# Kernel tuning notes

Measured on AMD Instinct MI355X. Metric: run time of the kernel, lower is better.

## Reference

```python
import jax, jax.numpy as jnp
import numpy as np

H = 64; DS = 32; DT = 24; ED = 16; OUT = 2
N = 10000       # nodes per type
E = 40000       # edges per edge type (before self loops)
MAX_DEG = 12    # static padded neighbor-sequence length (PyG to_dense_batch max); excess dropped


def setup_inputs() -> dict:
    key = jax.random.key(0)
    k = iter(jax.random.split(key, 40))
    def lin(o, i):
        s = 1.0 / np.sqrt(i)
        return jax.random.uniform(next(k), (o, i), jnp.float32, -s, s)
    inp = {}
    inp["x_source"] = jax.random.normal(next(k), (N, DS), jnp.float32)
    inp["x_target"] = jax.random.normal(next(k), (N, DT), jnp.float32)
    # 4 edge types in order [src->src, tgt->tgt, src->tgt, tgt->src], each [2, E]
    inp["edges"] = jax.random.randint(next(k), (4, 2, E), 0, N, dtype=jnp.int32)
    inp["edge_attr_st"] = jax.random.normal(next(k), (E, ED), jnp.float32)
    # node encoders (Linear-ReLU-Dropout(eval)-Linear)
    inp["We_s1"] = lin(H, DS); inp["be_s1"] = jnp.zeros((H,), jnp.float32)
    inp["We_s2"] = lin(H, H);  inp["be_s2"] = jnp.zeros((H,), jnp.float32)
    inp["We_t1"] = lin(H, DT); inp["be_t1"] = jnp.zeros((H,), jnp.float32)
    inp["We_t2"] = lin(H, H);  inp["be_t2"] = jnp.zeros((H,), jnp.float32)
    # 12 SAGEConv(aggr='lstm') blocks: 3 layers x 4 edge types, stacked on dim 0
    s = 1.0 / np.sqrt(H)
    inp["Wih"] = jax.random.uniform(next(k), (12, 4 * H, H), jnp.float32, -s, s)
    inp["Whh"] = jax.random.uniform(next(k), (12, 4 * H, H), jnp.float32, -s, s)
    inp["bih"] = jax.random.uniform(next(k), (12, 4 * H), jnp.float32, -s, s)
    inp["bhh"] = jax.random.uniform(next(k), (12, 4 * H), jnp.float32, -s, s)
    inp["Wl"]  = jax.random.uniform(next(k), (12, H, H), jnp.float32, -s, s)
    inp["bl"]  = jnp.zeros((12, H), jnp.float32)
    inp["Wr"]  = jax.random.uniform(next(k), (12, H, H), jnp.float32, -s, s)
    # edge gate + edge MLP head
    inp["Wg1"] = lin(H, 2 * H);   inp["bg1"] = jnp.zeros((H,), jnp.float32)
    inp["Wg2"] = lin(1, H);       inp["bg2"] = jnp.zeros((1,), jnp.float32)
    inp["Wm1"] = lin(H, H + ED);  inp["bm1"] = jnp.zeros((H,), jnp.float32)
    inp["Wm2"] = lin(H // 2, H);  inp["bm2"] = jnp.zeros((H // 2,), jnp.float32)
    inp["Wm3"] = lin(OUT, H // 2); inp["bm3"] = jnp.zeros((OUT,), jnp.float32)
    return inp


def _lstm_last(dense, Wih, Whh, bih, bhh):
    # dense: [n, T, H] padded neighbor sequences; PyG LSTMAggregation returns lstm(x)[0][:, -1]
    n = dense.shape[0]
    h0 = jnp.zeros((n, H), dense.dtype)
    def step(carry, x_t):
        h, c = carry
        g = x_t @ Wih.T + bih + h @ Whh.T + bhh  # torch gate order: i, f, g, o
        i, f, gg, o = jnp.split(g, 4, axis=-1)
        c = jax.nn.sigmoid(f) * c + jax.nn.sigmoid(i) * jnp.tanh(gg)
        h = jax.nn.sigmoid(o) * jnp.tanh(c)
        return (h, c), None
    (h, _), _ = jax.lax.scan(step, (h0, h0), jnp.swapaxes(dense, 0, 1))
    return h


def _sage_lstm(x_src, x_dst, src, dst, Wih, Whh, bih, bhh, Wl, bl, Wr):
    n_src, n_dst = x_src.shape[0], x_dst.shape[0]
    # add_self_loops(num_nodes=n_dst): appends (i, i) for every destination node, zero edge_attr
    loop = jnp.arange(n_dst, dtype=src.dtype)
    src = jnp.concatenate([src, loop]); dst = jnp.concatenate([dst, loop])
    # sort_edge_index(sort_by_row=False): stable lexicographic (dst, src) order
    order = jnp.argsort(dst.astype(jnp.int64) * n_src + src.astype(jnp.int64))
    src_s, dst_s = src[order], dst[order]
    xj = x_src[src_s]                                   # gather neighbor feats [E', H]
    deg = jnp.zeros((n_dst,), jnp.int32).at[dst_s].add(1)
    start = jnp.cumsum(deg) - deg                       # CSR row starts
    pos = jnp.arange(dst_s.shape[0], dtype=jnp.int32) - start[dst_s]
    dense = jnp.zeros((n_dst, MAX_DEG, x_src.shape[1]), x_src.dtype)
    dense = dense.at[dst_s, pos].set(xj, mode="drop")   # pad-to-dense, drop beyond MAX_DEG
    agg = _lstm_last(dense, Wih, Whh, bih, bhh)
    # SAGEConv: lin_l(aggr) + lin_r(x_root); lin_r has no bias
    return agg @ Wl.T + bl + x_dst @ Wr.T


def reference(x_source, x_target, edges, edge_attr_st,
              We_s1, be_s1, We_s2, be_s2, We_t1, be_t1, We_t2, be_t2,
              Wih, Whh, bih, bhh, Wl, bl, Wr,
              Wg1, bg1, Wg2, bg2, Wm1, bm1, Wm2, bm2, Wm3, bm3):
    relu = jax.nn.relu
    xs = relu(x_source @ We_s1.T + be_s1) @ We_s2.T + be_s2
    xt = relu(x_target @ We_t1.T + be_t1) @ We_t2.T + be_t2

    def layer(xs, xt, L):
        specs = [(xs, xs, 0), (xt, xt, 1), (xs, xt, 2), (xt, xs, 3)]
        outs = []
        for x_src, x_dst, et in specs:
            i = L * 4 + et
            outs.append(_sage_lstm(x_src, x_dst, edges[et, 0], edges[et, 1],
                                   Wih[i], Whh[i], bih[i], bhh[i], Wl[i], bl[i], Wr[i]))
        # HeteroConv(aggr='mean'): each node type receives from exactly 2 edge types
        return 0.5 * (outs[0] + outs[3]), 0.5 * (outs[1] + outs[2])

    s1, t1 = layer(xs, xt, 0); s1, t1 = relu(s1), relu(t1)
    s2, t2 = layer(s1, t1, 1); s2, t2 = relu(s2 + s1), relu(t2 + t1)
    s3, t3 = layer(s2, t2, 2); s3, t3 = relu(s3 + s2), relu(t3 + t2)

    # edge head on the main ('source','to','target') edges (original edges, no self loops)
    se, te = s3[edges[2, 0]], t3[edges[2, 1]]
    g = jax.nn.sigmoid(relu(jnp.concatenate([se, te], -1) @ Wg1.T + bg1) @ Wg2.T + bg2)
    er = g * se + (1.0 - g) * te
    h = relu(jnp.concatenate([er, edge_attr_st], -1) @ Wm1.T + bm1)
    h = relu(h @ Wm2.T + bm2)
    return h @ Wm3.T + bm3  # [E, OUT] edge logits
```

## Files before the change

kernel.cpp:

```cpp
#include <hip/hip_runtime.h>

#define N_NODES 10000
#define N_EDGES 40000
#define HD 64
#define MAXD 12
#define CAP 32
#define YROW ((size_t)(N_NODES + 1) * 256)
#define LOG2E 1.44269504f
#define XST 148

typedef __attribute__((ext_vector_type(8))) short short8;
typedef __attribute__((ext_vector_type(4))) float floatx4;

#define MFMA16(A, B, C) __builtin_amdgcn_mfma_f32_16x16x32_bf16(A, B, C, 0, 0, 0)

#if __has_builtin(__builtin_amdgcn_exp2f)
#define EXP2(x) __builtin_amdgcn_exp2f(x)
#else
#define EXP2(x) __expf((x) * 0.6931471806f)
#endif

__device__ __forceinline__ float sigmoidf_(float x) {
  return 1.0f / (1.0f + __expf(-x));
}
__device__ __forceinline__ float fma4(float4 w, float4 x, float a) {
  a = fmaf(w.x, x.x, a);
  a = fmaf(w.y, x.y, a);
  a = fmaf(w.z, x.z, a);
  return fmaf(w.w, x.w, a);
}

__device__ __forceinline__ void split_frag(float4 a, float4 b, short8& hi, short8& lo) {
  float f[8] = {a.x, a.y, a.z, a.w, b.x, b.y, b.z, b.w};
  union { short8 v; unsigned d[4]; } H, L;
#pragma unroll
  for (int p = 0; p < 4; ++p) {
    unsigned u0 = __float_as_uint(f[2 * p]);
    unsigned u1 = __float_as_uint(f[2 * p + 1]);
    H.d[p] = (u0 >> 16) | (u1 & 0xFFFF0000u);
    float l0 = f[2 * p] - __uint_as_float(u0 & 0xFFFF0000u);
    float l1 = f[2 * p + 1] - __uint_as_float(u1 & 0xFFFF0000u);
    L.d[p] = (__float_as_uint(l0) >> 16) | (__float_as_uint(l1) & 0xFFFF0000u);
  }
  hi = H.v;
  lo = L.v;
}


__global__ void scatter_kernel(const int* __restrict__ edges, int* __restrict__ cnt,
                               int* __restrict__ pool) {
  int idx = blockIdx.x * 256 + threadIdx.x;
  if (idx >= 4 * N_EDGES) return;
  int et = idx / N_EDGES, e = idx - et * N_EDGES;
  int src = edges[(et * 2) * N_EDGES + e];
  int dst = edges[(et * 2 + 1) * N_EDGES + e];
  int slot = atomicAdd(&cnt[et * N_NODES + dst], 1);
  if (slot < CAP) pool[(et * N_NODES + dst) * CAP + slot] = src;
}

__global__ void sortrows_kernel(const int* __restrict__ cnt, const int* __restrict__ pool,
                                int* __restrict__ nbr) {
  __shared__ int buf[64][CAP + 1];
  int idx = blockIdx.x * 64 + threadIdx.x;
  if (idx >= 4 * N_NODES) return;
  int n = idx % N_NODES;
  int c = cnt[idx];
  if (c > CAP) c = CAP;
  int* a = buf[threadIdx.x];
  const int* row = pool + idx * CAP;
  for (int j = 0; j < c; ++j) a[j] = row[j] * 2;
  a[c] = n * 2 + 1;
  ++c;
  for (int i2 = 1; i2 < c; ++i2) {
    int key = a[i2];
    int b = i2 - 1;
    while (b >= 0 && a[b] > key) { a[b + 1] = a[b]; --b; }
    a[b + 1] = key;
  }
  int* onbr = nbr + idx * MAXD;
  for (int t = 0; t < MAXD; ++t) onbr[t] = (t < c) ? (a[t] >> 1) : N_NODES;
}


__device__ __forceinline__ void wfrag_body(const float* __restrict__ W,
                                           short* __restrict__ w16, int gid) {
  int lane = gid & 63;
  int combo = gid >> 6;
  int kc = combo & 1;
  int g = (combo >> 1) & 3;
  int w = (combo >> 3) & 3;
  int i = combo >> 5;
  float sc = (g == 2) ? (2.0f * LOG2E) : LOG2E;
  int gate = g * 64 + w * 16 + (lane & 15);
  int k0 = kc * 32 + (lane >> 4) * 8;
  const float* src = W + ((size_t)i * 256 + gate) * 64 + k0;
  float4 a = ((const float4*)src)[0];
  float4 b = ((const float4*)src)[1];
  a.x *= sc; a.y *= sc; a.z *= sc; a.w *= sc;
  b.x *= sc; b.y *= sc; b.z *= sc; b.w *= sc;
  short8 hi, lo;
  split_frag(a, b, hi, lo);
  short8* dst = (short8*)w16;
  dst[(combo * 2 + 0) * 64 + lane] = hi;
  dst[(combo * 2 + 1) * 64 + lane] = lo;
}

__device__ __forceinline__ void cw_body(const float* __restrict__ Wl,
    const float* __restrict__ Wr, short* __restrict__ cw, int gid) {
  int lane = gid & 63;
  int rest = gid >> 6;
  int combo = rest & 7;
  int mat = (rest >> 3) % 3;
  int pair = rest / 24;
  int L = pair >> 1, side = pair & 1;
  int iA = L * 4 + (side ? 1 : 0);
  int iB = L * 4 + (side ? 2 : 3);
  int wp = combo >> 1, kc = combo & 1;
  int row = wp * 16 + (lane & 15);
  int k0 = kc * 32 + (lane >> 4) * 8;
  float4 a, b;
  if (mat == 0) {
    const float* s = Wl + ((size_t)iA * 64 + row) * 64 + k0;
    a = ((const float4*)s)[0]; b = ((const float4*)s)[1];
  } else if (mat == 1) {
    const float* s = Wl + ((size_t)iB * 64 + row) * 64 + k0;
    a = ((const float4*)s)[0]; b = ((const float4*)s)[1];
  } else {
    const float* sA = Wr + ((size_t)iA * 64 + row) * 64 + k0;
    const float* sB = Wr + ((size_t)iB * 64 + row) * 64 + k0;
    float4 a1 = ((const float4*)sA)[0], b1 = ((const float4*)sA)[1];
    float4 a2 = ((const float4*)sB)[0], b2 = ((const float4*)sB)[1];
    a.x = a1.x + a2.x; a.y = a1.y + a2.y; a.z = a1.z + a2.z; a.w = a1.w + a2.w;
    b.x = b1.x + b2.x; b.y = b1.y + b2.y; b.z = b1.z + b2.z; b.w = b1.w + b2.w;
  }
  short8 hi, lo;
  split_frag(a, b, hi, lo);
  short8* dst = (short8*)cw;
  int base = ((pair * 3 + mat) * 8 + combo) * 2;
  dst[(base + 0) * 64 + lane] = hi;
  dst[(base + 1) * 64 + lane] = lo;
}

__device__ __forceinline__ void eh_body(const float* __restrict__ Wg1,
    const float* __restrict__ Wm1, const float* __restrict__ Wm2,
    short* __restrict__ ehw16, int gid) {
  int lane = gid & 63;
  int combo = gid >> 6;
  int n = lane & 15, quad = lane >> 4;
  int mat, wp, kc;
  if (combo < 16) { mat = 0; wp = combo >> 2; kc = combo & 3; }
  else if (combo < 28) { int c2 = combo - 16; mat = 1; wp = c2 / 3; kc = c2 % 3; }
  else { int c2 = combo - 28; mat = 2; wp = c2 >> 1; kc = c2 & 1; }
  int row = wp * 16 + n;
  int k0 = kc * 32 + quad * 8;
  float4 a = {0.f, 0.f, 0.f, 0.f}, b = {0.f, 0.f, 0.f, 0.f};
  if (mat == 0) {
    const float* s = Wg1 + (size_t)row * 128 + k0;
    a = ((const float4*)s)[0]; b = ((const float4*)s)[1];
  } else if (mat == 1) {
    if (k0 + 8 <= 80) {
      const float* s = Wm1 + (size_t)row * 80 + k0;
      a = ((const float4*)s)[0]; b = ((const float4*)s)[1];
    }
  } else {
    const float* s = Wm2 + (size_t)row * 64 + k0;
    a = ((const float4*)s)[0]; b = ((const float4*)s)[1];
  }
  short8 hi, lo;
  split_frag(a, b, hi, lo);
  short8* dst = (short8*)ehw16;
  dst[(combo * 2 + 0) * 64 + lane] = hi;
  dst[(combo * 2 + 1) * 64 + lane] = lo;
}

__global__ __launch_bounds__(256) void prep_all_kernel(
    const float* __restrict__ Whh, const float* __restrict__ Wih,
    const float* __restrict__ Wl, const float* __restrict__ Wr,
    const float* __restrict__ Wg1, const float* __restrict__ Wm1,
    const float* __restrict__ Wm2,
    short* __restrict__ whh16, short* __restrict__ wih16, short* __restrict__ cw16,
    short* __restrict__ ehw16, float* __restrict__ ybase) {
  int gid = blockIdx.x * 256 + threadIdx.x;
  if (gid < 24576) {
    wfrag_body(Whh, whh16, gid);
  } else if (gid < 49152) {
    wfrag_body(Wih, wih16, gid - 24576);
  } else if (gid < 58368) {
    cw_body(Wl, Wr, cw16, gid - 49152);
  } else if (gid < 60416) {
    eh_body(Wg1, Wm1, Wm2, ehw16, gid - 58368);
  } else if (gid < 61440) {
    int t = gid - 60416;
    int et = t >> 8, col = t & 255;
    ybase[(size_t)et * YROW + (size_t)N_NODES * 256 + col] = 0.0f;
  }
}


template <int IN>
__device__ __forceinline__ void encode_body(const float* __restrict__ x,
    const float* __restrict__ W1, const float* __restrict__ b1,
    const float* __restrict__ W2, const float* __restrict__ b2, float* __restrict__ out) {
  __shared__ float xs[4][IN];
  __shared__ float h1[4][HD];
  int w = threadIdx.x >> 6, l = threadIdx.x & 63;
  int n = blockIdx.x * 4 + w;
  if (l < IN) xs[w][l] = x[n * IN + l];
  __syncthreads();
  float acc = b1[l];
#pragma unroll
  for (int k = 0; k < IN; ++k) acc = fmaf(xs[w][k], W1[l * IN + k], acc);
  h1[w][l] = fmaxf(acc, 0.0f);
  __syncthreads();
  float acc2 = b2[l];
#pragma unroll
  for (int k = 0; k < HD; ++k) acc2 = fmaf(h1[w][k], W2[l * HD + k], acc2);
  out[n * HD + l] = acc2;
}

__global__ __launch_bounds__(256) void encode_both_kernel(
    const float* __restrict__ xs0, const float* __restrict__ xt0,
    const float* __restrict__ Ws1, const float* __restrict__ bs1,
    const float* __restrict__ Ws2, const float* __restrict__ bs2,
    const float* __restrict__ Wt1, const float* __restrict__ bt1,
    const float* __restrict__ Wt2, const float* __restrict__ bt2,
    float* __restrict__ outS, float* __restrict__ outT) {
  if (blockIdx.y == 0) encode_body<32>(xs0, Ws1, bs1, Ws2, bs2, outS);
  else encode_body<24>(xt0, Wt1, bt1, Wt2, bt2, outT);
}


__global__ __launch_bounds__(256) void ygemm_mfma_kernel(const float* __restrict__ xs0,
    const float* __restrict__ xt0, const short* __restrict__ wih16L, float* __restrict__ ybase) {
  __shared__ __align__(16) float xS[16][68];
  __shared__ __align__(16) float pS[16][260];
  int et = blockIdx.y;
  const float* x = (et == 0 || et == 2) ? xs0 : xt0;
  const short8* wf = (const short8*)(wih16L + (size_t)et * 32768);
  float* y = ybase + (size_t)et * YROW;
  int tid = threadIdx.x, w = tid >> 6, l = tid & 63;
  int quad = l >> 4, n = l & 15;
  int n0 = blockIdx.x * 16;
  {
    int node = tid >> 4, f4 = tid & 15;
    float4 v = *(const float4*)(x + (size_t)(n0 + node) * 64 + f4 * 4);
    *(float4*)&xS[node][f4 * 4] = v;
  }
  short8 Bh[4][2], Bl[4][2];
#pragma unroll
  for (int wp = 0; wp < 4; ++wp)
#pragma unroll
    for (int kc = 0; kc < 2; ++kc) {
      int combo = (wp * 4 + w) * 2 + kc;
      Bh[wp][kc] = wf[(combo * 2 + 0) * 64 + l];
      Bl[wp][kc] = wf[(combo * 2 + 1) * 64 + l];
    }
  __syncthreads();
  short8 Ah[2], Al[2];
  {
    const float* hp = &xS[n][quad * 8];
    float4 q0 = *(const float4*)hp, q1 = *(const float4*)(hp + 4);
    float4 q2 = *(const float4*)(hp + 32), q3 = *(const float4*)(hp + 36);
    split_frag(q0, q1, Ah[0], Al[0]);
    split_frag(q2, q3, Ah[1], Al[1]);
  }
  floatx4 acc[4];
#pragma unroll
  for (int wp = 0; wp < 4; ++wp) {
    floatx4 a = {0.f, 0.f, 0.f, 0.f};
    a = MFMA16(Ah[0], Bh[wp][0], a);
    a = MFMA16(Ah[1], Bh[wp][1], a);
    a = MFMA16(Al[0], Bh[wp][0], a);
    a = MFMA16(Al[1], Bh[wp][1], a);
    a = MFMA16(Ah[0], Bl[wp][0], a);
    a = MFMA16(Ah[1], Bl[wp][1], a);
    acc[wp] = a;
  }
#pragma unroll
  for (int wp = 0; wp < 4; ++wp)
#pragma unroll
    for (int r = 0; r < 4; ++r)
      pS[quad * 4 + r][(wp * 16 + n) * 4 + w] = acc[wp][r];
  __syncthreads();
#pragma unroll
  for (int cc = 0; cc < 4; ++cc) {
    int g4 = cc * 256 + tid;
    int node = g4 >> 6, col = g4 & 63;
    float4 v = *(const float4*)&pS[node][col * 4];
    ((float4*)(y + (size_t)(n0 + node) * 256))[col] = v;
  }
}


__global__ __launch_bounds__(256) void lstm_mfma_kernel(const int* __restrict__ nbrAll,
    const float* __restrict__ ybase, const short* __restrict__ whh16L,
    const float* __restrict__ bihL, const float* __restrict__ bhhL, float* __restrict__ aggBase) {
  __shared__ __align__(16) unsigned pkS[2][16 * 68];
  __shared__ int nbS[16][MAXD];
  int et = blockIdx.y;
  const int* nbr = nbrAll + (size_t)et * N_NODES * MAXD;
  const float4* y4 = (const float4*)(ybase + (size_t)et * YROW);
  const short* whh16 = whh16L + (size_t)et * 32768;
  const float* bih = bihL + et * 256;
  const float* bhh = bhhL + et * 256;
  float* agg = aggBase + (size_t)et * N_NODES * HD;
  int tid = threadIdx.x, w = tid >> 6, l = tid & 63;
  int quad = l >> 4, n = l & 15, u = w * 16 + n;
  int n0 = blockIdx.x * 16;
  if (tid < 16 * MAXD) ((int*)nbS)[tid] = nbr[n0 * MAXD + tid];
  short8 Bh[4][2], Bl[4][2];
  {
    const short8* wf = (const short8*)whh16;
#pragma unroll
    for (int g = 0; g < 4; ++g)
#pragma unroll
      for (int kc = 0; kc < 2; ++kc) {
        int combo = (w * 4 + g) * 2 + kc;
        Bh[g][kc] = wf[(combo * 2 + 0) * 64 + l];
        Bl[g][kc] = wf[(combo * 2 + 1) * 64 + l];
      }
  }
  float bs[4];
#pragma unroll
  for (int g = 0; g < 4; ++g)
    bs[g] = (bih[g * 64 + u] + bhh[g * 64 + u]) * ((g == 2) ? (2.0f * LOG2E) : LOG2E);
  float c[4] = {0.f, 0.f, 0.f, 0.f}, h[4];
  short8 Ah[2], Al[2];
#pragma unroll
  for (int kc = 0; kc < 2; ++kc) { Ah[kc] = (short8)0; Al[kc] = (short8)0; }
  __syncthreads();
  float4 Y[4];
#pragma unroll
  for (int r = 0; r < 4; ++r) Y[r] = y4[(size_t)nbS[quad * 4 + r][0] * 64 + u];
  for (int t = 0; t < MAXD; ++t) {
    float yg[4][4];
#pragma unroll
    for (int r = 0; r < 4; ++r) {
      yg[0][r] = Y[r].x; yg[1][r] = Y[r].y; yg[2][r] = Y[r].z; yg[3][r] = Y[r].w;
    }
    floatx4 acc[4];
#pragma unroll
    for (int g = 0; g < 4; ++g) {
      floatx4 a = {yg[g][0], yg[g][1], yg[g][2], yg[g][3]};
      a = MFMA16(Ah[0], Bh[g][0], a);
      a = MFMA16(Ah[1], Bh[g][1], a);
      a = MFMA16(Al[0], Bh[g][0], a);
      a = MFMA16(Al[1], Bh[g][1], a);
      a = MFMA16(Ah[0], Bl[g][0], a);
      a = MFMA16(Ah[1], Bl[g][1], a);
      acc[g] = a;
    }
    if (t + 1 < MAXD) {
#pragma unroll
      for (int r = 0; r < 4; ++r) Y[r] = y4[(size_t)nbS[quad * 4 + r][t + 1] * 64 + u];
    }
    int buf = (t + 1) & 1;
#pragma unroll
    for (int r = 0; r < 4; ++r) {
      float gi = acc[0][r] + bs[0];
      float gf = acc[1][r] + bs[1];
      float gg = acc[2][r] + bs[2];
      float go = acc[3][r] + bs[3];
      float a_ = EXP2(-gi);
      float b_ = EXP2(fminf(-gg, 60.f));
      float f_ = EXP2(-gf);
      float o_ = EXP2(-go);
      float p1 = 1.f + a_, p2 = 1.f + b_, p3 = 1.f + f_;
      float d1 = p1 * p2;
      float num = fmaf(c[r], d1, (1.f - b_) * p3);
      c[r] = num * __builtin_amdgcn_rcpf(p3 * d1);
      float e_ = EXP2(c[r] * (-2.0f * LOG2E));
      h[r] = (1.f - e_) * __builtin_amdgcn_rcpf((1.f + e_) * (1.f + o_));
      unsigned ub = __float_as_uint(h[r]);
      float lo = h[r] - __uint_as_float(ub & 0xFFFF0000u);
      pkS[buf][(quad * 4 + r) * 68 + u] =
          __builtin_amdgcn_perm(ub, __float_as_uint(lo), 0x07060302u);
    }
    __syncthreads();
    if (t + 1 < MAXD) {
#pragma unroll
      for (int kc = 0; kc < 2; ++kc) {
        const unsigned* pb = &pkS[buf][n * 68 + kc * 32 + quad * 8];
        uint4 qa = *(const uint4*)pb;
        uint4 qb = *(const uint4*)(pb + 4);
        union { short8 s; unsigned d[4]; } H, L;
        H.d[0] = __builtin_amdgcn_perm(qa.y, qa.x, 0x07060302u);
        H.d[1] = __builtin_amdgcn_perm(qa.w, qa.z, 0x07060302u);
        H.d[2] = __builtin_amdgcn_perm(qb.y, qb.x, 0x07060302u);
        H.d[3] = __builtin_amdgcn_perm(qb.w, qb.z, 0x07060302u);
        L.d[0] = __builtin_amdgcn_perm(qa.y, qa.x, 0x05040100u);
        L.d[1] = __builtin_amdgcn_perm(qa.w, qa.z, 0x05040100u);
        L.d[2] = __builtin_amdgcn_perm(qb.y, qb.x, 0x05040100u);
        L.d[3] = __builtin_amdgcn_perm(qb.w, qb.z, 0x05040100u);
        Ah[kc] = H.s;
        Al[kc] = L.s;
      }
    }
  }
#pragma unroll
  for (int r = 0; r < 4; ++r)
    agg[(size_t)(n0 + quad * 4 + r) * HD + u] = h[r];
}


__global__ __launch_bounds__(256) void combine_mfma_kernel(const float* __restrict__ aggBase,
    const short* __restrict__ cwL, const float* __restrict__ blL,
    const float* __restrict__ xS0, const float* __restrict__ xT0, int has_res,
    float* __restrict__ outS, float* __restrict__ outT) {
  __shared__ __align__(16) float tS[3][16][68];
  int side = blockIdx.y;
  int etA = side ? 1 : 0, etB = side ? 2 : 3;
  const float* srcs[3];
  srcs[0] = aggBase + (size_t)etA * N_NODES * HD;
  srcs[1] = aggBase + (size_t)etB * N_NODES * HD;
  srcs[2] = side ? xT0 : xS0;
  float* out = side ? outT : outS;
  const short8* wf = (const short8*)cwL + (size_t)side * 3072;
  const float* blA = blL + etA * 64;
  const float* blB = blL + etB * 64;
  int tid = threadIdx.x, w = tid >> 6, l = tid & 63;
  int quad = l >> 4, n = l & 15;
  int n0 = blockIdx.x * 16;
  {
    int node = tid >> 4, f4 = tid & 15;
#pragma unroll
    for (int m = 0; m < 3; ++m) {
      float4 v = *(const float4*)(srcs[m] + (size_t)(n0 + node) * 64 + f4 * 4);
      *(float4*)&tS[m][node][f4 * 4] = v;
    }
  }
  short8 Bh[3][2], Bl[3][2];
#pragma unroll
  for (int m = 0; m < 3; ++m)
#pragma unroll
    for (int kc = 0; kc < 2; ++kc) {
      int base = (m * 8 + w * 2 + kc) * 2;
      Bh[m][kc] = wf[(base + 0) * 64 + l];
      Bl[m][kc] = wf[(base + 1) * 64 + l];
    }
  float bsum = blA[w * 16 + n] + blB[w * 16 + n];
  __syncthreads();
  floatx4 a = {0.f, 0.f, 0.f, 0.f};
#pragma unroll
  for (int m = 0; m < 3; ++m) {
    short8 Ah[2], Al[2];
    const float* hp = &tS[m][n][quad * 8];
    float4 q0 = *(const float4*)hp, q1 = *(const float4*)(hp + 4);
    float4 q2 = *(const float4*)(hp + 32), q3 = *(const float4*)(hp + 36);
    split_frag(q0, q1, Ah[0], Al[0]);
    split_frag(q2, q3, Ah[1], Al[1]);
    a = MFMA16(Ah[0], Bh[m][0], a);
    a = MFMA16(Ah[1], Bh[m][1], a);
    a = MFMA16(Al[0], Bh[m][0], a);
    a = MFMA16(Al[1], Bh[m][1], a);
    a = MFMA16(Ah[0], Bl[m][0], a);
    a = MFMA16(Ah[1], Bl[m][1], a);
  }
#pragma unroll
  for (int r = 0; r < 4; ++r) {
    int node = quad * 4 + r;
    float v = 0.5f * (a[r] + bsum);
    if (has_res) v += tS[2][node][w * 16 + n];
    out[(size_t)(n0 + node) * 64 + w * 16 + n] = fmaxf(v, 0.f);
  }
}


__global__ __launch_bounds__(256) void edge_head_mfma_kernel(
    const int* __restrict__ esrc, const int* __restrict__ edst, const float* __restrict__ ea,
    const float* __restrict__ s3, const float* __restrict__ t3,
    const short* __restrict__ ehw16,
    const float* __restrict__ bg1, const float* __restrict__ Wg2,
    const float* __restrict__ bg2, const float* __restrict__ bm1,
    const float* __restrict__ bm2, const float* __restrict__ Wm3,
    const float* __restrict__ bm3, float* __restrict__ out) {
  __shared__ __align__(16) float xS[64][XST];
  __shared__ float gP[4][64];
  int tid = threadIdx.x, w = tid >> 6, l = tid & 63;
  int quad = l >> 4, n = l & 15;
  int e0 = blockIdx.x * 64;
  const short8* wf = (const short8*)ehw16;
  for (int idx = tid; idx < 2048; idx += 256) {
    int e = idx >> 5, kk = idx & 31;
    float4 v;
    if (kk < 16) v = ((const float4*)(s3 + (size_t)esrc[e0 + e] * 64))[kk];
    else         v = ((const float4*)(t3 + (size_t)edst[e0 + e] * 64))[kk - 16];
    *(float4*)&xS[e][kk * 4] = v;
  }
  {
    int e = tid >> 2, kk = tid & 3;
    *(float4*)&xS[e][128 + kk * 4] = ((const float4*)(ea + (size_t)(e0 + e) * 16))[kk];
  }
  __syncthreads();
  {
    short8 Bh[4], Bl[4];
#pragma unroll
    for (int kc = 0; kc < 4; ++kc) {
      int cb = w * 4 + kc;
      Bh[kc] = wf[(cb * 2 + 0) * 64 + l];
      Bl[kc] = wf[(cb * 2 + 1) * 64 + l];
    }
    float bg = bg1[w * 16 + n];
    float wg2l = Wg2[w * 16 + n];
    float red[4][4];
#pragma unroll
    for (int mt = 0; mt < 4; ++mt) {
      floatx4 a = {bg, bg, bg, bg};
#pragma unroll
      for (int kc = 0; kc < 4; ++kc) {
        const float* hp = &xS[mt * 16 + n][kc * 32 + quad * 8];
        float4 q0 = *(const float4*)hp, q1 = *(const float4*)(hp + 4);
        short8 Ah, Al;
        split_frag(q0, q1, Ah, Al);
        a = MFMA16(Ah, Bh[kc], a);
        a = MFMA16(Al, Bh[kc], a);
        a = MFMA16(Ah, Bl[kc], a);
      }
#pragma unroll
      for (int r = 0; r < 4; ++r) red[mt][r] = fmaxf(a[r], 0.f) * wg2l;
    }
#pragma unroll
    for (int mt = 0; mt < 4; ++mt)
#pragma unroll
      for (int r = 0; r < 4; ++r) {
#pragma unroll
        for (int off = 1; off < 16; off <<= 1)
          red[mt][r] += __shfl_xor(red[mt][r], off);
      }
#pragma unroll
    for (int mt = 0; mt < 4; ++mt)
#pragma unroll
      for (int r = 0; r < 4; ++r)
        if (n == mt * 4 + r) gP[w][mt * 16 + quad * 4 + r] = red[mt][r];
  }
  __syncthreads();
  float gv[4];
  {
    float b2 = bg2[0];
#pragma unroll
    for (int mt = 0; mt < 4; ++mt) {
      int e = mt * 16 + n;
      float p = gP[0][e] + gP[1][e] + gP[2][e] + gP[3][e] + b2;
      gv[mt] = sigmoidf_(p);
    }
  }
  floatx4 acc2[4];
  {
    short8 Bh[3], Bl[3];
#pragma unroll
    for (int kc = 0; kc < 3; ++kc) {
      int cb = 16 + w * 3 + kc;
      Bh[kc] = wf[(cb * 2 + 0) * 64 + l];
      Bl[kc] = wf[(cb * 2 + 1) * 64 + l];
    }
    float bm = bm1[w * 16 + n];
#pragma unroll
    for (int mt = 0; mt < 4; ++mt) {
      int e = mt * 16 + n;
      float g = gv[mt];
      floatx4 a = {bm, bm, bm, bm};
#pragma unroll
      for (int kc = 0; kc < 2; ++kc) {
        const float* sp = &xS[e][kc * 32 + quad * 8];
        float4 s0 = *(const float4*)sp, s1 = *(const float4*)(sp + 4);
        float4 t0 = *(const float4*)(sp + 64), t1 = *(const float4*)(sp + 68);
        float4 e0v, e1v;
        e0v.x = fmaf(g, s0.x - t0.x, t0.x); e0v.y = fmaf(g, s0.y - t0.y, t0.y);
        e0v.z = fmaf(g, s0.z - t0.z, t0.z); e0v.w = fmaf(g, s0.w - t0.w, t0.w);
        e1v.x = fmaf(g, s1.x - t1.x, t1.x); e1v.y = fmaf(g, s1.y - t1.y, t1.y);
        e1v.z = fmaf(g, s1.z - t1.z, t1.z); e1v.w = fmaf(g, s1.w - t1.w, t1.w);
        short8 Ah, Al;
        split_frag(e0v, e1v, Ah, Al);
        a = MFMA16(Ah, Bh[kc], a);
        a = MFMA16(Al, Bh[kc], a);
        a = MFMA16(Ah, Bl[kc], a);
      }
      {
        float4 z0 = {0.f, 0.f, 0.f, 0.f}, z1 = {0.f, 0.f, 0.f, 0.f};
        if (quad < 2) {
          const float* ap = &xS[e][128 + quad * 8];
          z0 = *(const float4*)ap;
          z1 = *(const float4*)(ap + 4);
        }
        short8 Ah, Al;
        split_frag(z0, z1, Ah, Al);
        a = MFMA16(Ah, Bh[2], a);
        a = MFMA16(Al, Bh[2], a);
        a = MFMA16(Ah, Bl[2], a);
      }
      acc2[mt] = a;
    }
  }
  __syncthreads();
#pragma unroll
  for (int mt = 0; mt < 4; ++mt)
#pragma unroll
    for (int r = 0; r < 4; ++r)
      xS[mt * 16 + quad * 4 + r][w * 16 + n] = fmaxf(acc2[mt][r], 0.f);
  __syncthreads();
  {
    int s = w & 1, mtb = (w >> 1) * 2;
    short8 Bh[2], Bl[2];
#pragma unroll
    for (int kc = 0; kc < 2; ++kc) {
      int cb = 28 + s * 2 + kc;
      Bh[kc] = wf[(cb * 2 + 0) * 64 + l];
      Bl[kc] = wf[(cb * 2 + 1) * 64 + l];
    }
    float bm = bm2[s * 16 + n];
#pragma unroll
    for (int mi = 0; mi < 2; ++mi) {
      int mt = mtb + mi;
      int e = mt * 16 + n;
      floatx4 a = {bm, bm, bm, bm};
#pragma unroll
      for (int kc = 0; kc < 2; ++kc) {
        const float* sp = &xS[e][kc * 32 + quad * 8];
        float4 q0 = *(const float4*)sp, q1 = *(const float4*)(sp + 4);
        short8 Ah, Al;
        split_frag(q0, q1, Ah, Al);
        a = MFMA16(Ah, Bh[kc], a);
        a = MFMA16(Al, Bh[kc], a);
        a = MFMA16(Ah, Bl[kc], a);
      }
#pragma unroll
      for (int r = 0; r < 4; ++r)
        xS[mt * 16 + quad * 4 + r][64 + s * 16 + n] = fmaxf(a[r], 0.f);
    }
  }
  __syncthreads();
  if (tid < 128) {
    int e = tid >> 1, j = tid & 1;
    const float4* hp = (const float4*)&xS[e][64];
    const float4* w3 = (const float4*)(Wm3 + j * 32);
    float a = bm3[j];
#pragma unroll
    for (int kk = 0; kk < 8; ++kk) a = fma4(w3[kk], hp[kk], a);
    out[(e0 + e) * 2 + j] = a;
  }
}


extern "C" void kernel_launch(void* const* d_in, const int* in_sizes, int n_in, void* d_out,
                              int out_size, void* d_ws, size_t ws_size, hipStream_t stream) {
  const float* x_source = (const float*)d_in[0];
  const float* x_target = (const float*)d_in[1];
  const int* edges = (const int*)d_in[2];
  const float* edge_attr = (const float*)d_in[3];
  const float* We_s1 = (const float*)d_in[4];
  const float* be_s1 = (const float*)d_in[5];
  const float* We_s2 = (const float*)d_in[6];
  const float* be_s2 = (const float*)d_in[7];
  const float* We_t1 = (const float*)d_in[8];
  const float* be_t1 = (const float*)d_in[9];
  const float* We_t2 = (const float*)d_in[10];
  const float* be_t2 = (const float*)d_in[11];
  const float* Wih = (const float*)d_in[12];
  const float* Whh = (const float*)d_in[13];
  const float* bih = (const float*)d_in[14];
  const float* bhh = (const float*)d_in[15];
  const float* Wl = (const float*)d_in[16];
  const float* bl = (const float*)d_in[17];
  const float* Wr = (const float*)d_in[18];
  const float* Wg1 = (const float*)d_in[19];
  const float* bg1 = (const float*)d_in[20];
  const float* Wg2 = (const float*)d_in[21];
  const float* bg2 = (const float*)d_in[22];
  const float* Wm1 = (const float*)d_in[23];
  const float* bm1 = (const float*)d_in[24];
  const float* Wm2 = (const float*)d_in[25];
  const float* bm2 = (const float*)d_in[26];
  const float* Wm3 = (const float*)d_in[27];
  const float* bm3 = (const float*)d_in[28];
  float* out = (float*)d_out;

  int* nbr = (int*)d_ws;
  int* cnt = nbr + 4 * N_NODES * MAXD;
  int* pool = cnt + 4 * N_NODES;
  float* fb = (float*)(pool + 4 * N_NODES * CAP);
  float* bufS[2] = {fb, fb + N_NODES * HD};
  float* bufT[2] = {fb + 2 * N_NODES * HD, fb + 3 * N_NODES * HD};
  float* aggBase = fb + (size_t)4 * N_NODES * HD;
  float* y4 = fb + (size_t)8 * N_NODES * HD;
  short* whh16 = (short*)(y4 + 4 * YROW);
  short* wih16 = whh16 + 12 * 32768;
  short* cw16 = wih16 + 12 * 32768;
  short* ehw16 = cw16 + 6 * 24576;

  hipMemsetAsync(cnt, 0, 4 * N_NODES * sizeof(int), stream);
  prep_all_kernel<<<240, 256, 0, stream>>>(Whh, Wih, Wl, Wr, Wg1, Wm1, Wm2,
      whh16, wih16, cw16, ehw16, y4);
  scatter_kernel<<<(4 * N_EDGES + 255) / 256, 256, 0, stream>>>(edges, cnt, pool);
  sortrows_kernel<<<(4 * N_NODES + 63) / 64, 64, 0, stream>>>(cnt, pool, nbr);
  encode_both_kernel<<<dim3(N_NODES / 4, 2), 256, 0, stream>>>(x_source, x_target,
      We_s1, be_s1, We_s2, be_s2, We_t1, be_t1, We_t2, be_t2, bufS[0], bufT[0]);

  int cur = 0;
  for (int L = 0; L < 3; ++L) {
    ygemm_mfma_kernel<<<dim3(N_NODES / 16, 4), 256, 0, stream>>>(bufS[cur], bufT[cur],
        wih16 + (size_t)L * 4 * 32768, y4);
    lstm_mfma_kernel<<<dim3(N_NODES / 16, 4), 256, 0, stream>>>(nbr, y4,
        whh16 + (size_t)L * 4 * 32768, bih + L * 1024, bhh + L * 1024, aggBase);
    combine_mfma_kernel<<<dim3(N_NODES / 16, 2), 256, 0, stream>>>(aggBase,
        cw16 + (size_t)L * 2 * 24576, bl + L * 256,
        bufS[cur], bufT[cur], L > 0 ? 1 : 0, bufS[1 - cur], bufT[1 - cur]);
    cur = 1 - cur;
  }

  edge_head_mfma_kernel<<<N_EDGES / 64, 256, 0, stream>>>(edges + 4 * N_EDGES,
      edges + 5 * N_EDGES, edge_attr, bufS[cur], bufT[cur], ehw16,
      bg1, Wg2, bg2, bm1, bm2, Wm3, bm3, out);
}
```

Before: 444.4 us.

## Fuse next-layer input GEMM into combine and process 32 nodes per LSTM block

The combine kernel now also computes the next layer's LSTM input projection (x·Wih) for both edge types that read each node type, so the separate ygemm launches for layers 2 and 3 go away. This avoids rereading node features from global memory. The LSTM kernel handles two 16-node M-tiles per block, reusing the register-resident Whh fragments across 32 nodes, with the neighbor table padded to NPAD. The Wih fragment prep drops its scaling through a separate noscale path. The fused combine kernel uses more shared memory and registers, and the larger LSTM blocks halve the grid size.

```diff
diff --git a/kernel.cpp b/kernel.cpp
--- a/kernel.cpp
+++ b/kernel.cpp
@@ -1,6 +1,7 @@
 #include <hip/hip_runtime.h>
 
 #define N_NODES 10000
+#define NPAD 10016
 #define N_EDGES 40000
 #define HD 64
 #define MAXD 12
@@ -62,12 +63,17 @@
                                 int* __restrict__ nbr) {
   __shared__ int buf[64][CAP + 1];
   int idx = blockIdx.x * 64 + threadIdx.x;
-  if (idx >= 4 * N_NODES) return;
-  int n = idx % N_NODES;
-  int c = cnt[idx];
+  if (idx >= 4 * NPAD) return;
+  int et = idx / NPAD, n = idx - et * NPAD;
+  int* onbr = nbr + (size_t)idx * MAXD;
+  if (n >= N_NODES) {
+    for (int t = 0; t < MAXD; ++t) onbr[t] = N_NODES;
+    return;
+  }
+  int c = cnt[et * N_NODES + n];
   if (c > CAP) c = CAP;
   int* a = buf[threadIdx.x];
-  const int* row = pool + idx * CAP;
+  const int* row = pool + (size_t)(et * N_NODES + n) * CAP;
   for (int j = 0; j < c; ++j) a[j] = row[j] * 2;
   a[c] = n * 2 + 1;
   ++c;
@@ -77,7 +83,6 @@
     while (b >= 0 && a[b] > key) { a[b + 1] = a[b]; --b; }
     a[b + 1] = key;
   }
-  int* onbr = nbr + idx * MAXD;
   for (int t = 0; t < MAXD; ++t) onbr[t] = (t < c) ? (a[t] >> 1) : N_NODES;
 }
 
@@ -98,6 +103,26 @@
   float4 b = ((const float4*)src)[1];
   a.x *= sc; a.y *= sc; a.z *= sc; a.w *= sc;
   b.x *= sc; b.y *= sc; b.z *= sc; b.w *= sc;
+  short8 hi, lo;
+  split_frag(a, b, hi, lo);
+  short8* dst = (short8*)w16;
+  dst[(combo * 2 + 0) * 64 + lane] = hi;
+  dst[(combo * 2 + 1) * 64 + lane] = lo;
+}
+
+__device__ __forceinline__ void wfrag_body_noscale(const float* __restrict__ W,
+                                                   short* __restrict__ w16, int gid) {
+  int lane = gid & 63;
+  int combo = gid >> 6;
+  int kc = combo & 1;
+  int g = (combo >> 1) & 3;
+  int w = (combo >> 3) & 3;
+  int i = combo >> 5;
+  int gate = g * 64 + w * 16 + (lane & 15);
+  int k0 = kc * 32 + (lane >> 4) * 8;
+  const float* src = W + ((size_t)i * 256 + gate) * 64 + k0;
+  float4 a = ((const float4*)src)[0];
+  float4 b = ((const float4*)src)[1];
   short8 hi, lo;
   split_frag(a, b, hi, lo);
   short8* dst = (short8*)w16;
@@ -184,7 +209,7 @@
   if (gid < 24576) {
     wfrag_body(Whh, whh16, gid);
   } else if (gid < 49152) {
-    wfrag_body(Wih, wih16, gid - 24576);
+    wfrag_body_noscale(Wih, wih16, gid - 24576);
   } else if (gid < 58368) {
     cw_body(Wl, Wr, cw16, gid - 49152);
   } else if (gid < 60416) {
@@ -295,10 +320,10 @@
 __global__ __launch_bounds__(256) void lstm_mfma_kernel(const int* __restrict__ nbrAll,
     const float* __restrict__ ybase, const short* __restrict__ whh16L,
     const float* __restrict__ bihL, const float* __restrict__ bhhL, float* __restrict__ aggBase) {
-  __shared__ __align__(16) unsigned pkS[2][16 * 68];
-  __shared__ int nbS[16][MAXD];
+  __shared__ __align__(16) unsigned pkS[2][32 * 68];
+  __shared__ int nbS[32][MAXD];
   int et = blockIdx.y;
-  const int* nbr = nbrAll + (size_t)et * N_NODES * MAXD;
+  const int* nbr = nbrAll + (size_t)et * NPAD * MAXD;
   const float4* y4 = (const float4*)(ybase + (size_t)et * YROW);
   const short* whh16 = whh16L + (size_t)et * 32768;
   const float* bih = bihL + et * 256;
@@ -306,8 +331,8 @@
   float* agg = aggBase + (size_t)et * N_NODES * HD;
   int tid = threadIdx.x, w = tid >> 6, l = tid & 63;
   int quad = l >> 4, n = l & 15, u = w * 16 + n;
-  int n0 = blockIdx.x * 16;
-  if (tid < 16 * MAXD) ((int*)nbS)[tid] = nbr[n0 * MAXD + tid];
+  int n0 = blockIdx.x * 32;
+  for (int i = tid; i < 32 * MAXD; i += 256) ((int*)nbS)[i] = nbr[(size_t)n0 * MAXD + i];
   short8 Bh[4][2], Bl[4][2];
   {
     const short8* wf = (const short8*)whh16;
@@ -324,90 +349,105 @@
 #pragma unroll
   for (int g = 0; g < 4; ++g)
     bs[g] = (bih[g * 64 + u] + bhh[g * 64 + u]) * ((g == 2) ? (2.0f * LOG2E) : LOG2E);
-  float c[4] = {0.f, 0.f, 0.f, 0.f}, h[4];
-  short8 Ah[2], Al[2];
-#pragma unroll
-  for (int kc = 0; kc < 2; ++kc) { Ah[kc] = (short8)0; Al[kc] = (short8)0; }
-  __syncthreads();
-  float4 Y[4];
-#pragma unroll
-  for (int r = 0; r < 4; ++r) Y[r] = y4[(size_t)nbS[quad * 4 + r][0] * 64 + u];
+  float c[2][4] = {{0.f, 0.f, 0.f, 0.f}, {0.f, 0.f, 0.f, 0.f}}, h[2][4];
+  short8 Ah[2][2], Al[2][2];
+#pragma unroll
+  for (int mt = 0; mt < 2; ++mt)
+#pragma unroll
+    for (int kc = 0; kc < 2; ++kc) { Ah[mt][kc] = (short8)0; Al[mt][kc] = (short8)0; }
+  __syncthreads();
+  float4 Y[2][4];
+#pragma unroll
+  for (int mt = 0; mt < 2; ++mt)
+#pragma unroll
+    for (int r = 0; r < 4; ++r)
+      Y[mt][r] = y4[(size_t)nbS[mt * 16 + quad * 4 + r][0] * 64 + u];
   for (int t = 0; t < MAXD; ++t) {
-    float yg[4][4];
-#pragma unroll
-    for (int r = 0; r < 4; ++r) {
-      yg[0][r] = Y[r].x; yg[1][r] = Y[r].y; yg[2][r] = Y[r].z; yg[3][r] = Y[r].w;
-    }
-    floatx4 acc[4];
-#pragma unroll
-    for (int g = 0; g < 4; ++g) {
-      floatx4 a = {yg[g][0], yg[g][1], yg[g][2], yg[g][3]};
-      a = MFMA16(Ah[0], Bh[g][0], a);
-      a = MFMA16(Ah[1], Bh[g][1], a);
-      a = MFMA16(Al[0], Bh[g][0], a);
-      a = MFMA16(Al[1], Bh[g][1], a);
-      a = MFMA16(Ah[0], Bl[g][0], a);
-      a = MFMA16(Ah[1], Bl[g][1], a);
-      acc[g] = a;
-    }
+    floatx4 acc[2][4];
+#pragma unroll
+    for (int g = 0; g < 4; ++g)
+#pragma unroll
+      for (int mt = 0; mt < 2; ++mt) {
+        floatx4 a = {Y[mt][0][g], Y[mt][1][g], Y[mt][2][g], Y[mt][3][g]};
+        a = MFMA16(Ah[mt][0], Bh[g][0], a);
+        a = MFMA16(Ah[mt][1], Bh[g][1], a);
+        a = MFMA16(Al[mt][0], Bh[g][0], a);
+        a = MFMA16(Al[mt][1], Bh[g][1], a);
+        a = MFMA16(Ah[mt][0], Bl[g][0], a);
+        a = MFMA16(Ah[mt][1], Bl[g][1], a);
+        acc[mt][g] = a;
+      }
     if (t + 1 < MAXD) {
 #pragma unroll
-      for (int r = 0; r < 4; ++r) Y[r] = y4[(size_t)nbS[quad * 4 + r][t + 1] * 64 + u];
+      for (int mt = 0; mt < 2; ++mt)
+#pragma unroll
+        for (int r = 0; r < 4; ++r)
+          Y[mt][r] = y4[(size_t)nbS[mt * 16 + quad * 4 + r][t + 1] * 64 + u];
     }
     int buf = (t + 1) & 1;
 #pragma unroll
-    for (int r = 0; r < 4; ++r) {
-      float gi = acc[0][r] + bs[0];
-      float gf = acc[1][r] + bs[1];
-      float gg = acc[2][r] + bs[2];
-      float go = acc[3][r] + bs[3];
-      float a_ = EXP2(-gi);
-      float b_ = EXP2(fminf(-gg, 60.f));
-      float f_ = EXP2(-gf);
-      float o_ = EXP2(-go);
-      float p1 = 1.f + a_, p2 = 1.f + b_, p3 = 1.f + f_;
-      float d1 = p1 * p2;
-      float num = fmaf(c[r], d1, (1.f - b_) * p3);
-      c[r] = num * __builtin_amdgcn_rcpf(p3 * d1);
-      float e_ = EXP2(c[r] * (-2.0f * LOG2E));
-      h[r] = (1.f - e_) * __builtin_amdgcn_rcpf((1.f + e_) * (1.f + o_));
-      unsigned ub = __float_as_uint(h[r]);
-      float lo = h[r] - __uint_as_float(ub & 0xFFFF0000u);
-      pkS[buf][(quad * 4 + r) * 68 + u] =
-          __builtin_amdgcn_perm(ub, __float_as_uint(lo), 0x07060302u);
-    }
+    for (int mt = 0; mt < 2; ++mt)
+#pragma unroll
+      for (int r = 0; r < 4; ++r) {
+        float gi = acc[mt][0][r] + bs[0];
+        float gf = acc[mt][1][r] + bs[1];
+        float gg = acc[mt][2][r] + bs[2];
+        float go = acc[mt][3][r] + bs[3];
+        float a_ = EXP2(-gi);
+        float b_ = EXP2(fminf(-gg, 60.f));
+        float f_ = EXP2(-gf);
+        float o_ = EXP2(-go);
+        float p1 = 1.f + a_, p2 = 1.f + b_, p3 = 1.f + f_;
+        float d1 = p1 * p2;
+        float num = fmaf(c[mt][r], d1, (1.f - b_) * p3);
+        c[mt][r] = num * __builtin_amdgcn_rcpf(p3 * d1);
+        float e_ = EXP2(c[mt][r] * (-2.0f * LOG2E));
+        h[mt][r] = (1.f - e_) * __builtin_amdgcn_rcpf((1.f + e_) * (1.f + o_));
+        unsigned ub = __float_as_uint(h[mt][r]);
+        float lo = h[mt][r] - __uint_as_float(ub & 0xFFFF0000u);
+        pkS[buf][(mt * 16 + quad * 4 + r) * 68 + u] =
+            __builtin_amdgcn_perm(ub, __float_as_uint(lo), 0x07060302u);
+      }
     __syncthreads();
     if (t + 1 < MAXD) {
 #pragma unroll
-      for (int kc = 0; kc < 2; ++kc) {
-        const unsigned* pb = &pkS[buf][n * 68 + kc * 32 + quad * 8];
-        uint4 qa = *(const uint4*)pb;
-        uint4 qb = *(const uint4*)(pb + 4);
-        union { short8 s; unsigned d[4]; } H, L;
-        H.d[0] = __builtin_amdgcn_perm(qa.y, qa.x, 0x07060302u);
-        H.d[1] = __builtin_amdgcn_perm(qa.w, qa.z, 0x07060302u);
-        H.d[2] = __builtin_amdgcn_perm(qb.y, qb.x, 0x07060302u);
-        H.d[3] = __builtin_amdgcn_perm(qb.w, qb.z, 0x07060302u);
-        L.d[0] = __builtin_amdgcn_perm(qa.y, qa.x, 0x05040100u);
-        L.d[1] = __builtin_amdgcn_perm(qa.w, qa.z, 0x05040100u);
-        L.d[2] = __builtin_amdgcn_perm(qb.y, qb.x, 0x05040100u);
-        L.d[3] = __builtin_amdgcn_perm(qb.w, qb.z, 0x05040100u);
-        Ah[kc] = H.s;
-        Al[kc] = L.s;
-      }
-    }
-  }
-#pragma unroll
-  for (int r = 0; r < 4; ++r)
-    agg[(size_t)(n0 + quad * 4 + r) * HD + u] = h[r];
-}
-
-
-__global__ __launch_bounds__(256) void combine_mfma_kernel(const float* __restrict__ aggBase,
+      for (int mt = 0; mt < 2; ++mt)
+#pragma unroll
+        for (int kc = 0; kc < 2; ++kc) {
+          const unsigned* pb = &pkS[buf][(mt * 16 + n) * 68 + kc * 32 + quad * 8];
+          uint4 qa = *(const uint4*)pb;
+          uint4 qb = *(const uint4*)(pb + 4);
+          union { short8 s; unsigned d[4]; } H, L;
+          H.d[0] = __builtin_amdgcn_perm(qa.y, qa.x, 0x07060302u);
+          H.d[1] = __builtin_amdgcn_perm(qa.w, qa.z, 0x07060302u);
+          H.d[2] = __builtin_amdgcn_perm(qb.y, qb.x, 0x07060302u);
+          H.d[3] = __builtin_amdgcn_perm(qb.w, qb.z, 0x07060302u);
+          L.d[0] = __builtin_amdgcn_perm(qa.y, qa.x, 0x05040100u);
+          L.d[1] = __builtin_amdgcn_perm(qa.w, qa.z, 0x05040100u);
+          L.d[2] = __builtin_amdgcn_perm(qb.y, qb.x, 0x05040100u);
+          L.d[3] = __builtin_amdgcn_perm(qb.w, qb.z, 0x05040100u);
+          Ah[mt][kc] = H.s;
+          Al[mt][kc] = L.s;
+        }
+    }
+  }
+#pragma unroll
+  for (int mt = 0; mt < 2; ++mt)
+#pragma unroll
+    for (int r = 0; r < 4; ++r) {
+      int node = n0 + mt * 16 + quad * 4 + r;
+      if (node < N_NODES) agg[(size_t)node * HD + u] = h[mt][r];
+    }
+}
+
+
+__global__ __launch_bounds__(256) void combine_y_kernel(const float* __restrict__ aggBase,
     const short* __restrict__ cwL, const float* __restrict__ blL,
     const float* __restrict__ xS0, const float* __restrict__ xT0, int has_res,
-    float* __restrict__ outS, float* __restrict__ outT) {
+    float* __restrict__ outS, float* __restrict__ outT,
+    const short* __restrict__ wihNext, float* __restrict__ ybase, int do_y) {
   __shared__ __align__(16) float tS[3][16][68];
+  __shared__ __align__(16) float pS[16][260];
   int side = blockIdx.y;
   int etA = side ? 1 : 0, etB = side ? 2 : 3;
   const float* srcs[3];
@@ -456,12 +496,62 @@
     a = MFMA16(Ah[0], Bl[m][0], a);
     a = MFMA16(Ah[1], Bl[m][1], a);
   }
+  __syncthreads();
 #pragma unroll
   for (int r = 0; r < 4; ++r) {
     int node = quad * 4 + r;
     float v = 0.5f * (a[r] + bsum);
     if (has_res) v += tS[2][node][w * 16 + n];
-    out[(size_t)(n0 + node) * 64 + w * 16 + n] = fmaxf(v, 0.f);
+    v = fmaxf(v, 0.f);
+    out[(size_t)(n0 + node) * 64 + w * 16 + n] = v;
+    tS[0][node][w * 16 + n] = v;
+  }
+  if (!do_y) return;
+  __syncthreads();
+  short8 Ah[2], Al[2];
+  {
+    const float* hp = &tS[0][n][quad * 8];
+    float4 q0 = *(const float4*)hp, q1 = *(const float4*)(hp + 4);
+    float4 q2 = *(const float4*)(hp + 32), q3 = *(const float4*)(hp + 36);
+    split_frag(q0, q1, Ah[0], Al[0]);
+    split_frag(q2, q3, Ah[1], Al[1]);
+  }
+#pragma unroll
+  for (int ei = 0; ei < 2; ++ei) {
+    int et = side ? (ei ? 3 : 1) : (ei ? 2 : 0);
+    const short8* wf2 = (const short8*)(wihNext + (size_t)et * 32768);
+    float* y = ybase + (size_t)et * YROW;
+    floatx4 acc[4];
+#pragma unroll
+    for (int wp = 0; wp < 4; ++wp) {
+      int combo = (wp * 4 + w) * 2;
+      short8 B0h = wf2[(combo * 2 + 0) * 64 + l];
+      short8 B0l = wf2[(combo * 2 + 1) * 64 + l];
+      short8 B1h = wf2[(combo * 2 + 2) * 64 + l];
+      short8 B1l = wf2[(combo * 2 + 3) * 64 + l];
+      floatx4 aa = {0.f, 0.f, 0.f, 0.f};
+      aa = MFMA16(Ah[0], B0h, aa);
+      aa = MFMA16(Ah[1], B1h, aa);
+      aa = MFMA16(Al[0], B0h, aa);
+      aa = MFMA16(Al[1], B1h, aa);
+      aa = MFMA16(Ah[0], B0l, aa);
+      aa = MFMA16(Ah[1], B1l, aa);
+      acc[wp] = aa;
+    }
+#pragma unroll
+    for (int wp = 0; wp < 4; ++wp)
+#pragma unroll
+      for (int r = 0; r < 4; ++r)
+        pS[quad * 4 + r][(wp * 16 + n) * 4 + w] = acc[wp][r];
+    __syncthreads();
+#pragma unroll
+    for (int cc = 0; cc < 4; ++cc) {
+      int g4 = cc * 256 + tid;
+      int node = g4 >> 6, col = g4 & 63;
+      float4 v = *(const float4*)&pS[node][col * 4];
+      ((float4*)(y + (size_t)(n0 + node) * 256))[col] = v;
+    }
+    if (ei == 0) __syncthreads();
   }
 }
 
@@ -675,7 +765,7 @@
   float* out = (float*)d_out;
 
   int* nbr = (int*)d_ws;
-  int* cnt = nbr + 4 * N_NODES * MAXD;
+  int* cnt = nbr + 4 * NPAD * MAXD;
   int* pool = cnt + 4 * N_NODES;
   float* fb = (float*)(pool + 4 * N_NODES * CAP);
   float* bufS[2] = {fb, fb + N_NODES * HD};
@@ -691,19 +781,19 @@
   prep_all_kernel<<<240, 256, 0, stream>>>(Whh, Wih, Wl, Wr, Wg1, Wm1, Wm2,
       whh16, wih16, cw16, ehw16, y4);
   scatter_kernel<<<(4 * N_EDGES + 255) / 256, 256, 0, stream>>>(edges, cnt, pool);
-  sortrows_kernel<<<(4 * N_NODES + 63) / 64, 64, 0, stream>>>(cnt, pool, nbr);
+  sortrows_kernel<<<(4 * NPAD + 63) / 64, 64, 0, stream>>>(cnt, pool, nbr);
   encode_both_kernel<<<dim3(N_NODES / 4, 2), 256, 0, stream>>>(x_source, x_target,
       We_s1, be_s1, We_s2, be_s2, We_t1, be_t1, We_t2, be_t2, bufS[0], bufT[0]);
 
+  ygemm_mfma_kernel<<<dim3(N_NODES / 16, 4), 256, 0, stream>>>(bufS[0], bufT[0], wih16, y4);
   int cur = 0;
   for (int L = 0; L < 3; ++L) {
-    ygemm_mfma_kernel<<<dim3(N_NODES / 16, 4), 256, 0, stream>>>(bufS[cur], bufT[cur],
-        wih16 + (size_t)L * 4 * 32768, y4);
-    lstm_mfma_kernel<<<dim3(N_NODES / 16, 4), 256, 0, stream>>>(nbr, y4,
+    lstm_mfma_kernel<<<dim3(NPAD / 32, 4), 256, 0, stream>>>(nbr, y4,
         whh16 + (size_t)L * 4 * 32768, bih + L * 1024, bhh + L * 1024, aggBase);
-    combine_mfma_kernel<<<dim3(N_NODES / 16, 2), 256, 0, stream>>>(aggBase,
+    combine_y_kernel<<<dim3(N_NODES / 16, 2), 256, 0, stream>>>(aggBase,
         cw16 + (size_t)L * 2 * 24576, bl + L * 256,
-        bufS[cur], bufT[cur], L > 0 ? 1 : 0, bufS[1 - cur], bufT[1 - cur]);
+        bufS[cur], bufT[cur], L > 0 ? 1 : 0, bufS[1 - cur], bufT[1 - cur],
+        wih16 + (size_t)(L < 2 ? (L + 1) : 0) * 4 * 32768, y4, L < 2 ? 1 : 0);
     cur = 1 - cur;
   }
 
```

Result: slower. 467.9 us (+5.3%).
